# Optimization experiments

Measured on AMD Instinct MI355X. Metric: run time of the kernel, lower is better.

The kernel has to match this reference:

```python
import jax, jax.numpy as jnp
import numpy as np

H, W = 720, 1280  # hardcoded in the original layer

def setup_inputs() -> dict:
    key = jax.random.key(0)
    k1, k2 = jax.random.split(key)
    feature_map = jax.random.normal(k1, (1, H, W, 64), dtype=jnp.float32)
    matrix = jax.random.normal(k2, (1, 3, 3), dtype=jnp.float32)  # ignored (overwritten) in forward, kept for fidelity
    return {"feature_map": feature_map, "matrix": matrix}

def reference(feature_map, matrix):
    B = feature_map.shape[0]  # must be 1 (reshape constraint in original)
    # Original overwrites `matrix` with a constant identity homography.
    M = jnp.eye(3, dtype=jnp.float32).reshape(1, 3, 3)
    # tf.meshgrid default 'xy' indexing: xx, yy have shape [W, H]
    xx, yy = jnp.meshgrid(jnp.arange(H), jnp.arange(W))
    xx_flat = xx.reshape(-1)
    yy_flat = yy.reshape(-1)
    homo = jnp.ones_like(xx_flat)
    grid = jnp.stack([xx_flat, yy_flat, homo]).astype(jnp.float32)  # [3, H*W]
    tg = jnp.matmul(M, grid).reshape(B, 3, H, W)  # [B,3,H,W]
    x_samples = jnp.floor(tg[:, 0] / tg[:, 2]).astype(jnp.int32)  # [B,H,W], values in [0,H)
    y_samples = jnp.floor(tg[:, 1] / tg[:, 2]).astype(jnp.int32)  # [B,H,W], values in [0,W)
    b = jnp.broadcast_to(jnp.arange(B, dtype=jnp.int32)[:, None, None], (B, H, W))
    # tf.gather_nd(feature_map, stack([b, x, y], -1)) == advanced indexing
    return feature_map[b, x_samples, y_samples]  # [B,H,W,C]
```

## Files before the change

### kernel.cpp

```cpp
#include <hip/hip_runtime.h>


#define HH 720
#define WW 1280
#define CC 64
#define V4 (CC / 4)
#define TOTAL4 (HH * WW * V4)

__global__ __launch_bounds__(256) void vtl_gather_kernel(
    const float4* __restrict__ in, float4* __restrict__ out) {
    int idx = blockIdx.x * blockDim.x + threadIdx.x;
    if (idx >= TOTAL4) return;
    int k = idx >> 4;
    int j = idx & 15;
    int x = k % HH;
    int y = k / HH;
    int s = x * WW + y;
    out[idx] = in[s * V4 + j];
}

extern "C" void kernel_launch(void* const* d_in, const int* in_sizes, int n_in,
                              void* d_out, int out_size, void* d_ws, size_t ws_size,
                              hipStream_t stream) {
    const float4* in = (const float4*)d_in[0];
    float4* out = (float4*)d_out;
    constexpr int threads = 256;
    constexpr int blocks = TOTAL4 / threads;
    vtl_gather_kernel<<<blocks, threads, 0, stream>>>(in, out);
}
```

Baseline: 94.97 us.

## Transpose via 16x16 LDS tiles with direct global-to-LDS async loads

Replaces the per-float4 gather with a tiled transpose. Each block stages a 16x16 pixel tile of 64 channels into shared memory with global_load_lds, then writes out the transposed rows. The aim is to make both the reads and the writes contiguous and to skip the register round trip on loads. The cost is 64KB of LDS per block, which limits occupancy, and a full-block barrier between the load and store phases.

```diff
diff --git a/kernel.cpp b/kernel.cpp
--- a/kernel.cpp
+++ b/kernel.cpp
@@ -3,28 +3,51 @@
 
 #define HH 720
 #define WW 1280
-#define CC 64
-#define V4 (CC / 4)
-#define TOTAL4 (HH * WW * V4)
+#define TX 16
+#define TY 16
+#define NTX (HH / TX)
+#define NTY (WW / TY)
 
-__global__ __launch_bounds__(256) void vtl_gather_kernel(
-    const float4* __restrict__ in, float4* __restrict__ out) {
-    int idx = blockIdx.x * blockDim.x + threadIdx.x;
-    if (idx >= TOTAL4) return;
-    int k = idx >> 4;
-    int j = idx & 15;
-    int x = k % HH;
-    int y = k / HH;
-    int s = x * WW + y;
-    out[idx] = in[s * V4 + j];
+__global__ __launch_bounds__(256) void vtl_tile_kernel(
+    const float* __restrict__ in, float4* __restrict__ out) {
+  __shared__ float4 lds[TX * TY * 16];
+
+  const int tile = blockIdx.x;
+  const int tx = tile % NTX;
+  const int ty = tile / NTX;
+  const int x0 = tx * TX;
+  const int y0 = ty * TY;
+  const int wave = threadIdx.x >> 6;
+  const int lane = threadIdx.x & 63;
+
+  for (int r = 0; r < 4; ++r) {
+    const int xr = wave * 4 + r;
+    const float* grow = in + ((size_t)(x0 + xr) * WW + y0) * 64;
+    float4* lbase = &lds[xr * 256];
+    for (int c = 0; c < 4; ++c) {
+      __builtin_amdgcn_global_load_lds(
+          (const __attribute__((address_space(1))) void*)(grow + (size_t)(c * 64 + lane) * 4),
+          (__attribute__((address_space(3))) void*)(lbase + c * 64),
+          16, 0, 0);
+    }
+  }
+  __syncthreads();
+
+  for (int r = 0; r < 4; ++r) {
+    const int yr = wave * 4 + r;
+    float4* gout = out + ((size_t)(y0 + yr) * HH + x0) * 16;
+    for (int c = 0; c < 4; ++c) {
+      const int x = c * 4 + (lane >> 4);
+      gout[c * 64 + lane] = lds[x * 256 + yr * 16 + (lane & 15)];
+    }
+  }
 }
 
 extern "C" void kernel_launch(void* const* d_in, const int* in_sizes, int n_in,
                               void* d_out, int out_size, void* d_ws, size_t ws_size,
                               hipStream_t stream) {
-    const float4* in = (const float4*)d_in[0];
-    float4* out = (float4*)d_out;
-    constexpr int threads = 256;
-    constexpr int blocks = TOTAL4 / threads;
-    vtl_gather_kernel<<<blocks, threads, 0, stream>>>(in, out);
+  const float* in = (const float*)d_in[0];
+  float4* out = (float4*)d_out;
+  constexpr int blocks = NTX * NTY;
+  vtl_tile_kernel<<<blocks, 256, 0, stream>>>(in, out);
 }
```

Measured after the change: 94.36 us. No clear change (-0.6%).
